# Kernel tuning notes

Hardware: AMD Instinct MI355X
Metric: run time of the kernel (lower is better)

The kernel has to match this reference:

```python
import jax, jax.numpy as jnp
import numpy as np

N_NODES = 50000
N_EDGES = 800000
D_IN = 128
D_OUT = 128


def setup_inputs() -> dict:
    key = jax.random.key(0)
    k1, k2, k3, k4, k5 = jax.random.split(key, 5)
    feature = jax.random.normal(k1, (N_NODES, D_IN), dtype=jnp.float32)
    src = jax.random.randint(k2, (N_EDGES,), 0, N_NODES, dtype=jnp.int32)
    dst = jax.random.randint(k3, (N_EDGES,), 0, N_NODES, dtype=jnp.int32)
    # nn.Linear default init scale ~ 1/sqrt(in_feats)
    W = jax.random.normal(k4, (D_OUT, D_IN), dtype=jnp.float32) / np.sqrt(D_IN)
    b = jax.random.normal(k5, (D_OUT,), dtype=jnp.float32) / np.sqrt(D_IN)
    return {"feature": feature, "src": src, "dst": dst, "W": W, "b": b}


def reference(feature, src, dst, W, b):
    # update_all(copy_src, sum): gather source node features per edge,
    # scatter-add into destination nodes -> [N, D_IN]
    msgs = feature[src]  # [E, D_IN]
    agg = jax.ops.segment_sum(msgs, dst, num_segments=N_NODES)
    # apply_nodes: linear + activation
    z = jax.nn.relu(agg @ W.T + b)
    # residual: in_feats == out_feats -> identity down path
    return z + feature
```

## Files before the change

kernel.cpp:

```cpp
#include <hip/hip_runtime.h>

#define N_NODES 50000
#define N_EDGES 800000
#define D 128
#define CAP 64

typedef unsigned short ushort_t;
typedef unsigned int uint_t;

#define WS_COUNTS 0
#define WS_ESRC   50048
#define WS_FB16   (WS_ESRC + N_NODES*CAP)
#define WS_FULL_BYTES  ((size_t)(WS_FB16 + N_NODES * D / 2) * 4)
#define WS_CSR_BYTES   ((size_t)(WS_ESRC + N_NODES * CAP) * 4)

__global__ __launch_bounds__(256) void tobf16_kernel(
    const float* __restrict__ f, ushort_t* __restrict__ fb) {
  const int i = blockIdx.x * 256 + threadIdx.x;
  if (i < N_NODES * D / 8) {
    const float4 v0 = ((const float4*)f)[2 * i];
    const float4 v1 = ((const float4*)f)[2 * i + 1];
    const float vs[8] = {v0.x, v0.y, v0.z, v0.w, v1.x, v1.y, v1.z, v1.w};
    ushort_t r[8];
#pragma unroll
    for (int k = 0; k < 8; ++k) {
      const uint_t u = __builtin_bit_cast(uint_t, vs[k]);
      r[k] = (ushort_t)((u + 0x7fffu + ((u >> 16) & 1u)) >> 16);
    }
    *(uint4*)(fb + (size_t)i * 8) = *(const uint4*)r;
  }
}

__global__ __launch_bounds__(256) void build_kernel(const int* __restrict__ src,
                                                    const int* __restrict__ dst,
                                                    int* __restrict__ counts,
                                                    int* __restrict__ esrc) {
  const int e = blockIdx.x * 256 + threadIdx.x;
  if (e < N_EDGES) {
    const int d = dst[e];
    const int pos = atomicAdd(&counts[d], 1);
    if (pos < CAP) esrc[(size_t)d * CAP + pos] = src[e];
  }
}

#define RPB 32
__global__ __launch_bounds__(256) void gather_transform_kernel(
    const float* __restrict__ feature,
    const ushort_t* __restrict__ fb16,
    const int* __restrict__ counts,
    const int* __restrict__ esrc,
    const float* __restrict__ W,
    const float* __restrict__ b,
    float* __restrict__ out) {
  __shared__ float sA[RPB][D];

  const int tid  = threadIdx.x;
  const int row0 = blockIdx.x * RPB;
  const int l = tid & 15;
  const int g = tid >> 4;

#pragma unroll
  for (int p = 0; p < 2; ++p) {
    const int r   = p * 16 + g;
    const int row = row0 + r;
    float a[8];
#pragma unroll
    for (int k = 0; k < 8; ++k) a[k] = 0.f;
    if (row < N_NODES) {
      int cnt = counts[row];
      if (cnt > CAP) cnt = CAP;
      const size_t base = (size_t)row * CAP;
      for (int j0 = 0; j0 < cnt; j0 += 16) {
        int eid = 0;
        if (j0 + l < cnt) eid = esrc[base + j0 + l];
        const int lim = (cnt - j0 < 16) ? (cnt - j0) : 16;
        if (lim == 16) {
#pragma unroll
          for (int k = 0; k < 16; ++k) {
            const int s = __shfl(eid, k, 16);
            const uint4 w4 = *(const uint4*)(fb16 + (size_t)s * D + l * 8);
            const uint_t ws[4] = {w4.x, w4.y, w4.z, w4.w};
#pragma unroll
            for (int q = 0; q < 4; ++q) {
              a[2 * q]     += __builtin_bit_cast(float, ws[q] << 16);
              a[2 * q + 1] += __builtin_bit_cast(float, ws[q] & 0xffff0000u);
            }
          }
        } else {
          for (int k = 0; k < lim; ++k) {
            const int s = __shfl(eid, k, 16);
            const uint4 w4 = *(const uint4*)(fb16 + (size_t)s * D + l * 8);
            const uint_t ws[4] = {w4.x, w4.y, w4.z, w4.w};
#pragma unroll
            for (int q = 0; q < 4; ++q) {
              a[2 * q]     += __builtin_bit_cast(float, ws[q] << 16);
              a[2 * q + 1] += __builtin_bit_cast(float, ws[q] & 0xffff0000u);
            }
          }
        }
      }
    }
    float4* sp = (float4*)&sA[r][l * 8];
    sp[0] = make_float4(a[0], a[1], a[2], a[3]);
    sp[1] = make_float4(a[4], a[5], a[6], a[7]);
  }
  __syncthreads();

  const int c  = tid & 127;
  const int rh = tid >> 7;

  float acc[16];
#pragma unroll
  for (int r = 0; r < 16; ++r) acc[r] = 0.f;

  for (int k = 0; k < D; ++k) {
    const float wv = W[c * D + k];
#pragma unroll
    for (int r = 0; r < 16; ++r)
      acc[r] += sA[rh * 16 + r][k] * wv;
  }

  const float bias = b[c];
#pragma unroll
  for (int r = 0; r < 16; ++r) {
    const int row = row0 + rh * 16 + r;
    if (row < N_NODES) {
      const size_t o = (size_t)row * D + c;
      float z = acc[r] + bias;
      z = z > 0.f ? z : 0.f;
      out[o] = z + feature[o];
    }
  }
}

__global__ __launch_bounds__(256) void gather_transform_f32_kernel(
    const float* __restrict__ feature,
    const int* __restrict__ counts,
    const int* __restrict__ esrc,
    const float* __restrict__ W,
    const float* __restrict__ b,
    float* __restrict__ out) {
  __shared__ float sA[RPB][D];
  const int tid  = threadIdx.x;
  const int row0 = blockIdx.x * RPB;
  const int l = tid & 15;
  const int g = tid >> 4;
#pragma unroll
  for (int p = 0; p < 2; ++p) {
    const int r   = p * 16 + g;
    const int row = row0 + r;
    float4 a0 = make_float4(0.f, 0.f, 0.f, 0.f);
    float4 a1 = make_float4(0.f, 0.f, 0.f, 0.f);
    if (row < N_NODES) {
      int cnt = counts[row];
      if (cnt > CAP) cnt = CAP;
      const size_t base = (size_t)row * CAP;
      for (int j0 = 0; j0 < cnt; j0 += 16) {
        int eid = 0;
        if (j0 + l < cnt) eid = esrc[base + j0 + l];
        const int lim = (cnt - j0 < 16) ? (cnt - j0) : 16;
        for (int k = 0; k < lim; ++k) {
          const int s = __shfl(eid, k, 16);
          const float* fp = feature + (size_t)s * D + l * 8;
          const float4 v0 = *(const float4*)fp;
          const float4 v1 = *(const float4*)(fp + 4);
          a0.x += v0.x; a0.y += v0.y; a0.z += v0.z; a0.w += v0.w;
          a1.x += v1.x; a1.y += v1.y; a1.z += v1.z; a1.w += v1.w;
        }
      }
    }
    float4* sp = (float4*)&sA[r][l * 8];
    sp[0] = a0; sp[1] = a1;
  }
  __syncthreads();
  const int c  = tid & 127;
  const int rh = tid >> 7;
  float acc[16];
#pragma unroll
  for (int r = 0; r < 16; ++r) acc[r] = 0.f;
  for (int k = 0; k < D; ++k) {
    const float wv = W[c * D + k];
#pragma unroll
    for (int r = 0; r < 16; ++r) acc[r] += sA[rh * 16 + r][k] * wv;
  }
  const float bias = b[c];
#pragma unroll
  for (int r = 0; r < 16; ++r) {
    const int row = row0 + rh * 16 + r;
    if (row < N_NODES) {
      const size_t o = (size_t)row * D + c;
      float z = acc[r] + bias;
      z = z > 0.f ? z : 0.f;
      out[o] = z + feature[o];
    }
  }
}

__global__ __launch_bounds__(256) void scatter_kernel(
    const float* __restrict__ feature,
    const int* __restrict__ src,
    const int* __restrict__ dst,
    float* __restrict__ agg) {
  const long long total = (long long)N_EDGES * (D / 4);
  long long idx = (long long)blockIdx.x * blockDim.x + threadIdx.x;
  const long long stride = (long long)gridDim.x * blockDim.x;
  for (; idx < total; idx += stride) {
    const int e  = (int)(idx >> 5);
    const int c4 = ((int)idx & 31) * 4;
    const float4 v = *(const float4*)(feature + (long long)src[e] * D + c4);
    float* p = agg + (long long)dst[e] * D + c4;
    atomicAdd(p + 0, v.x);
    atomicAdd(p + 1, v.y);
    atomicAdd(p + 2, v.z);
    atomicAdd(p + 3, v.w);
  }
}

__global__ __launch_bounds__(256) void transform_kernel(
    float* __restrict__ agg_out,
    const float* __restrict__ feature,
    const float* __restrict__ W,
    const float* __restrict__ b) {
  __shared__ float sA[RPB][D];
  const int row0 = blockIdx.x * RPB;
  for (int i = threadIdx.x; i < RPB * (D / 4); i += 256) {
    const int r  = i >> 5;
    const int c4 = (i & 31) * 4;
    const int row = row0 + r;
    float4 v = make_float4(0.f, 0.f, 0.f, 0.f);
    if (row < N_NODES) v = *(const float4*)(agg_out + (long long)row * D + c4);
    *(float4*)&sA[r][c4] = v;
  }
  __syncthreads();
  const int c  = threadIdx.x & 127;
  const int rh = threadIdx.x >> 7;
  float acc[16];
#pragma unroll
  for (int r = 0; r < 16; ++r) acc[r] = 0.f;
  for (int k = 0; k < D; ++k) {
    const float wv = W[c * D + k];
#pragma unroll
    for (int r = 0; r < 16; ++r) acc[r] += sA[rh * 16 + r][k] * wv;
  }
  const float bias = b[c];
#pragma unroll
  for (int r = 0; r < 16; ++r) {
    const int row = row0 + rh * 16 + r;
    if (row < N_NODES) {
      const long long o = (long long)row * D + c;
      float z = acc[r] + bias;
      z = z > 0.f ? z : 0.f;
      agg_out[o] = z + feature[o];
    }
  }
}

extern "C" void kernel_launch(void* const* d_in, const int* in_sizes, int n_in,
                              void* d_out, int out_size, void* d_ws, size_t ws_size,
                              hipStream_t stream) {
  const float* feature = (const float*)d_in[0];
  const int*   src     = (const int*)d_in[1];
  const int*   dst     = (const int*)d_in[2];
  const float* W       = (const float*)d_in[3];
  const float* b       = (const float*)d_in[4];
  float* out = (float*)d_out;

  const int eblocks = (N_EDGES + 255) / 256;
  const int nblocks = (N_NODES + RPB - 1) / RPB;

  if (ws_size >= WS_FULL_BYTES) {
    int*      wsi    = (int*)d_ws;
    int*      counts = wsi + WS_COUNTS;
    int*      esrc   = wsi + WS_ESRC;
    ushort_t* fb16   = (ushort_t*)(wsi + WS_FB16);

    hipMemsetAsync(counts, 0, (size_t)N_NODES * 4, stream);
    tobf16_kernel<<<(N_NODES * D / 8 + 255) / 256, 256, 0, stream>>>(feature, fb16);
    build_kernel<<<eblocks, 256, 0, stream>>>(src, dst, counts, esrc);
    gather_transform_kernel<<<nblocks, 256, 0, stream>>>(feature, fb16, counts,
                                                         esrc, W, b, out);
  } else if (ws_size >= WS_CSR_BYTES) {
    int* wsi    = (int*)d_ws;
    int* counts = wsi + WS_COUNTS;
    int* esrc   = wsi + WS_ESRC;

    hipMemsetAsync(counts, 0, (size_t)N_NODES * 4, stream);
    build_kernel<<<eblocks, 256, 0, stream>>>(src, dst, counts, esrc);
    gather_transform_f32_kernel<<<nblocks, 256, 0, stream>>>(feature, counts,
                                                             esrc, W, b, out);
  } else {
    hipMemsetAsync(out, 0, (size_t)N_NODES * D * sizeof(float), stream);
    scatter_kernel<<<2048, 256, 0, stream>>>(feature, src, dst, out);
    transform_kernel<<<nblocks, 256, 0, stream>>>(out, feature, W, b);
  }
}
```

Before: 211.9 us.

## Use bf16 MFMA for node transform and fuse prep with counts reset

Replaces the scalar FP32 per-thread dense transform with bf16 MFMA 16x16x32 instructions. The aggregated rows are packed from padded shared memory into bf16 fragments, and W is pre-converted to bf16 in workspace. The feature bf16 conversion, W conversion and counts zeroing are merged into one prep kernel, which removes the memset launch. This lowers ALU and issue cost in the GEMM phase, at the price of reduced precision from rounding the aggregates and weights to bf16.

```diff
diff --git a/kernel.cpp b/kernel.cpp
--- a/kernel.cpp
+++ b/kernel.cpp
@@ -7,28 +7,50 @@
 
 typedef unsigned short ushort_t;
 typedef unsigned int uint_t;
+typedef __attribute__((ext_vector_type(8))) short bf16x8;
+typedef __attribute__((ext_vector_type(4))) float f32x4;
 
 #define WS_COUNTS 0
 #define WS_ESRC   50048
 #define WS_FB16   (WS_ESRC + N_NODES*CAP)
-#define WS_FULL_BYTES  ((size_t)(WS_FB16 + N_NODES * D / 2) * 4)
+#define WS_WB16   (WS_FB16 + N_NODES*D/2)
+#define WS_FULL_BYTES  ((size_t)(WS_WB16 + D * D / 2) * 4)
 #define WS_CSR_BYTES   ((size_t)(WS_ESRC + N_NODES * CAP) * 4)
 
-__global__ __launch_bounds__(256) void tobf16_kernel(
-    const float* __restrict__ f, ushort_t* __restrict__ fb) {
+__device__ inline uint_t pack2bf16(float lo, float hi) {
+  uint_t ulo = __builtin_bit_cast(uint_t, lo);
+  uint_t uhi = __builtin_bit_cast(uint_t, hi);
+  ulo = (ulo + 0x7fffu + ((ulo >> 16) & 1u)) >> 16;
+  uhi = (uhi + 0x7fffu + ((uhi >> 16) & 1u)) & 0xffff0000u;
+  return ulo | uhi;
+}
+
+__global__ __launch_bounds__(256) void prep_kernel(
+    const float* __restrict__ f, const float* __restrict__ W,
+    int* __restrict__ counts, ushort_t* __restrict__ fb,
+    ushort_t* __restrict__ wb) {
   const int i = blockIdx.x * 256 + threadIdx.x;
   if (i < N_NODES * D / 8) {
     const float4 v0 = ((const float4*)f)[2 * i];
     const float4 v1 = ((const float4*)f)[2 * i + 1];
-    const float vs[8] = {v0.x, v0.y, v0.z, v0.w, v1.x, v1.y, v1.z, v1.w};
-    ushort_t r[8];
-#pragma unroll
-    for (int k = 0; k < 8; ++k) {
-      const uint_t u = __builtin_bit_cast(uint_t, vs[k]);
-      r[k] = (ushort_t)((u + 0x7fffu + ((u >> 16) & 1u)) >> 16);
-    }
+    uint_t r[4];
+    r[0] = pack2bf16(v0.x, v0.y);
+    r[1] = pack2bf16(v0.z, v0.w);
+    r[2] = pack2bf16(v1.x, v1.y);
+    r[3] = pack2bf16(v1.z, v1.w);
     *(uint4*)(fb + (size_t)i * 8) = *(const uint4*)r;
   }
+  if (i < D * D / 8) {
+    const float4 v0 = ((const float4*)W)[2 * i];
+    const float4 v1 = ((const float4*)W)[2 * i + 1];
+    uint_t r[4];
+    r[0] = pack2bf16(v0.x, v0.y);
+    r[1] = pack2bf16(v0.z, v0.w);
+    r[2] = pack2bf16(v1.x, v1.y);
+    r[3] = pack2bf16(v1.z, v1.w);
+    *(uint4*)(wb + (size_t)i * 8) = *(const uint4*)r;
+  }
+  if (i < 50048) counts[i] = 0;
 }
 
 __global__ __launch_bounds__(256) void build_kernel(const int* __restrict__ src,
@@ -47,12 +69,12 @@
 __global__ __launch_bounds__(256) void gather_transform_kernel(
     const float* __restrict__ feature,
     const ushort_t* __restrict__ fb16,
+    const ushort_t* __restrict__ wb16,
     const int* __restrict__ counts,
     const int* __restrict__ esrc,
-    const float* __restrict__ W,
     const float* __restrict__ b,
     float* __restrict__ out) {
-  __shared__ float sA[RPB][D];
+  __shared__ float sA[RPB][D + 4];
 
   const int tid  = threadIdx.x;
   const int row0 = blockIdx.x * RPB;
@@ -106,29 +128,59 @@
   }
   __syncthreads();
 
-  const int c  = tid & 127;
-  const int rh = tid >> 7;
-
-  float acc[16];
-#pragma unroll
-  for (int r = 0; r < 16; ++r) acc[r] = 0.f;
-
-  for (int k = 0; k < D; ++k) {
-    const float wv = W[c * D + k];
-#pragma unroll
-    for (int r = 0; r < 16; ++r)
-      acc[r] += sA[rh * 16 + r][k] * wv;
-  }
-
-  const float bias = b[c];
-#pragma unroll
-  for (int r = 0; r < 16; ++r) {
-    const int row = row0 + rh * 16 + r;
-    if (row < N_NODES) {
-      const size_t o = (size_t)row * D + c;
-      float z = acc[r] + bias;
-      z = z > 0.f ? z : 0.f;
-      out[o] = z + feature[o];
+  const int wave = tid >> 6;
+  const int lane = tid & 63;
+  const int lr = lane & 15;
+  const int lk = lane >> 4;
+
+  f32x4 acc00 = {0.f, 0.f, 0.f, 0.f}, acc01 = acc00;
+  f32x4 acc10 = acc00, acc11 = acc00;
+
+#pragma unroll
+  for (int ks = 0; ks < 4; ++ks) {
+    bf16x8 afr[2];
+#pragma unroll
+    for (int mt = 0; mt < 2; ++mt) {
+      const float* ap = &sA[mt * 16 + lr][ks * 32 + lk * 8];
+      const float4 a0 = *(const float4*)ap;
+      const float4 a1 = *(const float4*)(ap + 4);
+      uint_t u[4];
+      u[0] = pack2bf16(a0.x, a0.y);
+      u[1] = pack2bf16(a0.z, a0.w);
+      u[2] = pack2bf16(a1.x, a1.y);
+      u[3] = pack2bf16(a1.z, a1.w);
+      afr[mt] = __builtin_bit_cast(bf16x8, *(const uint4*)u);
+    }
+    bf16x8 bfr[2];
+#pragma unroll
+    for (int ntl = 0; ntl < 2; ++ntl) {
+      const int col = (2 * wave + ntl) * 16 + lr;
+      bfr[ntl] = *(const bf16x8*)(wb16 + (size_t)col * D + ks * 32 + lk * 8);
+    }
+    acc00 = __builtin_amdgcn_mfma_f32_16x16x32_bf16(afr[0], bfr[0], acc00, 0, 0, 0);
+    acc01 = __builtin_amdgcn_mfma_f32_16x16x32_bf16(afr[0], bfr[1], acc01, 0, 0, 0);
+    acc10 = __builtin_amdgcn_mfma_f32_16x16x32_bf16(afr[1], bfr[0], acc10, 0, 0, 0);
+    acc11 = __builtin_amdgcn_mfma_f32_16x16x32_bf16(afr[1], bfr[1], acc11, 0, 0, 0);
+  }
+
+#pragma unroll
+  for (int mt = 0; mt < 2; ++mt) {
+#pragma unroll
+    for (int ntl = 0; ntl < 2; ++ntl) {
+      const f32x4 av = (mt == 0) ? (ntl == 0 ? acc00 : acc01)
+                                 : (ntl == 0 ? acc10 : acc11);
+      const int col = (2 * wave + ntl) * 16 + lr;
+      const float bias = b[col];
+#pragma unroll
+      for (int j = 0; j < 4; ++j) {
+        const int row = row0 + mt * 16 + lk * 4 + j;
+        if (row < N_NODES) {
+          const size_t o = (size_t)row * D + col;
+          float z = av[j] + bias;
+          z = z > 0.f ? z : 0.f;
+          out[o] = z + feature[o];
+        }
+      }
     }
   }
 }
@@ -273,12 +325,12 @@
     int*      counts = wsi + WS_COUNTS;
     int*      esrc   = wsi + WS_ESRC;
     ushort_t* fb16   = (ushort_t*)(wsi + WS_FB16);
-
-    hipMemsetAsync(counts, 0, (size_t)N_NODES * 4, stream);
-    tobf16_kernel<<<(N_NODES * D / 8 + 255) / 256, 256, 0, stream>>>(feature, fb16);
+    ushort_t* wb16   = (ushort_t*)(wsi + WS_WB16);
+
+    prep_kernel<<<eblocks, 256, 0, stream>>>(feature, W, counts, fb16, wb16);
     build_kernel<<<eblocks, 256, 0, stream>>>(src, dst, counts, esrc);
-    gather_transform_kernel<<<nblocks, 256, 0, stream>>>(feature, fb16, counts,
-                                                         esrc, W, b, out);
+    gather_transform_kernel<<<nblocks, 256, 0, stream>>>(feature, fb16, wb16,
+                                                         counts, esrc, b, out);
   } else if (ws_size >= WS_CSR_BYTES) {
     int* wsi    = (int*)d_ws;
     int* counts = wsi + WS_COUNTS;
```

After: 189.0 us. -10.8%, faster.
